# Performance work log

Measured on AMD Instinct MI355X. Metric: run time of the kernel, lower is better.

## Reference

```python
import jax, jax.numpy as jnp
import numpy as np

N_NODES = 50000
N_EDGES = 800000
IN_FEATS = 128
N_HIDDEN = 64
OUT_FEATS = 40
DIM = 8  # pseudo-coordinate dimension
K = 1    # n_kernels


def setup_inputs() -> dict:
    key = jax.random.key(0)
    ks = jax.random.split(key, 12)
    inp = {
        "features": jax.random.normal(ks[0], (N_NODES, IN_FEATS), dtype=jnp.float32),
        "edge_weight": jax.random.normal(ks[1], (N_EDGES, DIM), dtype=jnp.float32),
        "src": jax.random.randint(ks[2], (N_EDGES,), 0, N_NODES),
        "dst": jax.random.randint(ks[3], (N_EDGES,), 0, N_NODES),
        # layer 1 params (fc has no bias in DGL GMMConv; separate additive bias)
        "W1": jax.random.normal(ks[4], (IN_FEATS, K * N_HIDDEN), dtype=jnp.float32) * (1.0 / np.sqrt(IN_FEATS)),
        "b1": jnp.zeros((N_HIDDEN,), dtype=jnp.float32),
        "mu1": jax.random.normal(ks[5], (K, DIM), dtype=jnp.float32) * 0.1,
        "inv_sigma1": jnp.ones((K, DIM), dtype=jnp.float32),
        # layer 2 params
        "W2": jax.random.normal(ks[6], (N_HIDDEN, K * OUT_FEATS), dtype=jnp.float32) * (1.0 / np.sqrt(N_HIDDEN)),
        "b2": jnp.zeros((OUT_FEATS,), dtype=jnp.float32),
        "mu2": jax.random.normal(ks[7], (K, DIM), dtype=jnp.float32) * 0.1,
        "inv_sigma2": jnp.ones((K, DIM), dtype=jnp.float32),
    }
    return inp


def gmm_conv(x, pseudo, src, dst, W, b, mu, inv_sigma, out_feats):
    # x: [N, in], pseudo: [E, DIM], W: [in, K*out]
    h = (x @ W).reshape(-1, K, out_feats)                      # [N, K, out]
    # gaussian mixture weights per edge/kernel: [E, K]
    diff = pseudo[:, None, :] - mu[None, :, :]                 # [E, K, DIM]
    gw = jnp.exp(-0.5 * jnp.sum(diff * diff * (inv_sigma[None] ** 2), axis=-1))
    # gather src feats, weight, sum over kernels: [E, out]
    msg = jnp.einsum("ekf,ek->ef", h[src], gw)
    agg = jax.ops.segment_sum(msg, dst, num_segments=N_NODES)  # [N, out]
    return agg + b


def reference(features, edge_weight, src, dst, W1, b1, mu1, inv_sigma1, W2, b2, mu2, inv_sigma2):
    x = gmm_conv(features, edge_weight, src, dst, W1, b1, mu1, inv_sigma1, N_HIDDEN)
    x = gmm_conv(x, edge_weight, src, dst, W2, b2, mu2, inv_sigma2, OUT_FEATS)
    return jax.nn.log_softmax(x, axis=1)
```

## Files before the change

kernel.cpp:

```cpp
#include <hip/hip_runtime.h>
#include <hip/hip_fp16.h>
#include <math.h>

#define N_NODES 50000
#define N_EDGES 800000
#define IN_FEATS 128
#define N_HIDDEN 64
#define OUT_FEATS 40
#define DIM 8
#define GT_TILES ((N_NODES + 63) / 64)
#define HIST_NB ((N_EDGES / 4 + 255) / 256)
#define FILL_BLOCKS (N_EDGES / 256)
#define SCAN_NB ((N_NODES + 255) / 256)
#define CNT_STRIDE 4

typedef _Float16 half8 __attribute__((ext_vector_type(8)));
typedef float floatx4 __attribute__((ext_vector_type(4)));

__device__ __forceinline__ int wave_incl_scan(int x, int lane) {
#pragma unroll
    for (int off = 1; off < 64; off <<= 1) {
        int v = __shfl_up(x, off, 64);
        if (lane >= off) x += v;
    }
    return x;
}

__global__ __launch_bounds__(256) void histgemm_kernel(
    const float* __restrict__ features, const float* __restrict__ W1,
    const int* __restrict__ dst,
    int* __restrict__ counts, unsigned short* __restrict__ rank,
    __half* __restrict__ h1)
{
    const int tid = threadIdx.x;
    __shared__ __align__(16) __half WT[64][136];

    if (blockIdx.x < HIST_NB) {
        int i = blockIdx.x * 256 + tid;
        if (i * 4 >= N_EDGES) return;
        int4 d = ((const int4*)dst)[i];
        ushort4 r;
        r.x = (unsigned short)atomicAdd(&counts[d.x * CNT_STRIDE], 1);
        r.y = (unsigned short)atomicAdd(&counts[d.y * CNT_STRIDE], 1);
        r.z = (unsigned short)atomicAdd(&counts[d.z * CNT_STRIDE], 1);
        r.w = (unsigned short)atomicAdd(&counts[d.w * CNT_STRIDE], 1);
        ((ushort4*)rank)[i] = r;
        return;
    }

    int nodeBase = (blockIdx.x - HIST_NB) * 64;
    for (int rep = 0; rep < 32; ++rep) {
        int idx = tid + rep * 256;
        int k = idx >> 6, n = idx & 63;
        WT[n][k] = __float2half(W1[idx]);
    }
    __syncthreads();

    int lane = tid & 63, w = tid >> 6;
    int m = lane & 15, quad = lane >> 4;
    int row = nodeBase + w * 16 + m;
    int rowc = (row < N_NODES) ? row : (N_NODES - 1);
    const float* fr = features + (size_t)rowc * IN_FEATS;

    floatx4 acc0 = {0.f,0.f,0.f,0.f}, acc1 = acc0, acc2 = acc0, acc3 = acc0;
#pragma unroll
    for (int kc = 0; kc < 4; ++kc) {
        float4 fa = *(const float4*)(fr + kc * 32 + quad * 8);
        float4 fb = *(const float4*)(fr + kc * 32 + quad * 8 + 4);
        union { half8 v; __half2 h2[4]; } A;
        A.h2[0] = __floats2half2_rn(fa.x, fa.y);
        A.h2[1] = __floats2half2_rn(fa.z, fa.w);
        A.h2[2] = __floats2half2_rn(fb.x, fb.y);
        A.h2[3] = __floats2half2_rn(fb.z, fb.w);
        half8 b0 = *(const half8*)&WT[ 0 + m][kc * 32 + quad * 8];
        half8 b1 = *(const half8*)&WT[16 + m][kc * 32 + quad * 8];
        half8 b2 = *(const half8*)&WT[32 + m][kc * 32 + quad * 8];
        half8 b3 = *(const half8*)&WT[48 + m][kc * 32 + quad * 8];
        acc0 = __builtin_amdgcn_mfma_f32_16x16x32_f16(A.v, b0, acc0, 0, 0, 0);
        acc1 = __builtin_amdgcn_mfma_f32_16x16x32_f16(A.v, b1, acc1, 0, 0, 0);
        acc2 = __builtin_amdgcn_mfma_f32_16x16x32_f16(A.v, b2, acc2, 0, 0, 0);
        acc3 = __builtin_amdgcn_mfma_f32_16x16x32_f16(A.v, b3, acc3, 0, 0, 0);
    }
    int nodeRow = nodeBase + w * 16 + quad * 4;
#pragma unroll
    for (int r = 0; r < 4; ++r) {
        int n = nodeRow + r;
        if (n < N_NODES) {
            size_t base = (size_t)n * N_HIDDEN + m;
            h1[base +  0] = __float2half(acc0[r]);
            h1[base + 16] = __float2half(acc1[r]);
            h1[base + 32] = __float2half(acc2[r]);
            h1[base + 48] = __float2half(acc3[r]);
        }
    }
}

__global__ __launch_bounds__(256) void scan_partial_kernel(const int* __restrict__ counts,
                                                           int* __restrict__ offsets,
                                                           int* __restrict__ partials) {
    const int tid = threadIdx.x, bid = blockIdx.x;
    const int i = bid * 256 + tid;
    const int lane = tid & 63, wid = tid >> 6;
    int x = (i < N_NODES) ? counts[i * CNT_STRIDE] : 0;
    int incl = wave_incl_scan(x, lane);
    __shared__ int wsum[4];
    if (lane == 63) wsum[wid] = incl;
    __syncthreads();
    int base = 0;
#pragma unroll
    for (int w = 0; w < 4; ++w)
        if (w < wid) base += wsum[w];
    if (i < N_NODES) offsets[i] = base + incl - x;
    if (tid == 255) partials[bid] = base + incl;
}

__global__ __launch_bounds__(256) void scan_base_kernel(int* __restrict__ partials) {
    const int tid = threadIdx.x;
    const int lane = tid & 63, wid = tid >> 6;
    int x = (tid < SCAN_NB) ? partials[tid] : 0;
    int incl = wave_incl_scan(x, lane);
    __shared__ int wsum[4];
    if (lane == 63) wsum[wid] = incl;
    __syncthreads();
    int base = 0;
#pragma unroll
    for (int w = 0; w < 4; ++w)
        if (w < wid) base += wsum[w];
    if (tid < SCAN_NB) partials[tid] = base + incl - x;
}

__global__ __launch_bounds__(256) void scan_add_kernel(int* __restrict__ offsets,
                                                       const int* __restrict__ partials) {
    const int i = blockIdx.x * 256 + threadIdx.x;
    if (i < N_NODES) offsets[i] += partials[blockIdx.x];
    if (i == N_NODES) offsets[N_NODES] = N_EDGES;
}

__global__ __launch_bounds__(256) void fill_kernel(
    const int* __restrict__ src, const int* __restrict__ dst,
    const float* __restrict__ ew,
    const float* __restrict__ mu1, const float* __restrict__ is1,
    const float* __restrict__ mu2, const float* __restrict__ is2,
    const int* __restrict__ offsets, const unsigned short* __restrict__ rank,
    int2* __restrict__ csr)
{
    int e = blockIdx.x * 256 + threadIdx.x;
    int sN = src[e];
    int dN = dst[e];
    unsigned short rk = rank[e];
    const float4* ew4 = (const float4*)(ew + (size_t)e * DIM);
    float4 wa = ew4[0], wb = ew4[1];
    float v[8] = {wa.x, wa.y, wa.z, wa.w, wb.x, wb.y, wb.z, wb.w};
    float s1 = 0.f, s2 = 0.f;
#pragma unroll
    for (int d = 0; d < DIM; ++d) {
        float d1 = v[d] - mu1[d]; float a1 = is1[d];
        float d2 = v[d] - mu2[d]; float a2 = is2[d];
        s1 += d1 * d1 * a1 * a1;
        s2 += d2 * d2 * a2 * a2;
    }
    __half2 g = __floats2half2_rn(expf(-0.5f * s1), expf(-0.5f * s2));
    int2 rec;
    rec.x = sN;
    rec.y = *reinterpret_cast<int*>(&g);
    int pos = offsets[dN] + rk;
    __builtin_nontemporal_store(*reinterpret_cast<long long*>(&rec),
                                reinterpret_cast<long long*>(&csr[pos]));
}

__global__ __launch_bounds__(256) void agg1_gemm2_kernel(const __half* __restrict__ h,
                                                         const int* __restrict__ offsets,
                                                         const int2* __restrict__ csr,
                                                         const float* __restrict__ b,
                                                         const float* __restrict__ W2,
                                                         __half* __restrict__ h2) {
    __shared__ float xs[8][64];
    const unsigned* h32 = (const unsigned*)h;
    const int tid = threadIdx.x;
    const int w = tid >> 6, lane = tid & 63;
    const int hf = lane >> 5, p = lane & 31;
    const int ln = w * 2 + hf;
    const int n = blockIdx.x * 8 + ln;
    int beg = offsets[n], end = offsets[n + 1];

    float ax = 0.f, ay = 0.f;
    for (int j = beg; j < end; j += 8) {
        int j0 = j + 0, j1 = j + 1, j2 = j + 2, j3 = j + 3;
        int j4 = j + 4, j5 = j + 5, j6 = j + 6, j7 = j + 7;
        int e1 = end - 1;
        int2 r0 = csr[(j0 < end) ? j0 : e1];
        int2 r1 = csr[(j1 < end) ? j1 : e1];
        int2 r2 = csr[(j2 < end) ? j2 : e1];
        int2 r3 = csr[(j3 < end) ? j3 : e1];
        int2 r4 = csr[(j4 < end) ? j4 : e1];
        int2 r5 = csr[(j5 < end) ? j5 : e1];
        int2 r6 = csr[(j6 < end) ? j6 : e1];
        int2 r7 = csr[(j7 < end) ? j7 : e1];
        unsigned v0 = h32[(size_t)r0.x * 32 + p];
        unsigned v1 = h32[(size_t)r1.x * 32 + p];
        unsigned v2 = h32[(size_t)r2.x * 32 + p];
        unsigned v3 = h32[(size_t)r3.x * 32 + p];
        unsigned v4 = h32[(size_t)r4.x * 32 + p];
        unsigned v5 = h32[(size_t)r5.x * 32 + p];
        unsigned v6 = h32[(size_t)r6.x * 32 + p];
        unsigned v7 = h32[(size_t)r7.x * 32 + p];
        float g0 = (j0 < end) ? __low2float(*reinterpret_cast<__half2*>(&r0.y)) : 0.f;
        float g1 = (j1 < end) ? __low2float(*reinterpret_cast<__half2*>(&r1.y)) : 0.f;
        float g2 = (j2 < end) ? __low2float(*reinterpret_cast<__half2*>(&r2.y)) : 0.f;
        float g3 = (j3 < end) ? __low2float(*reinterpret_cast<__half2*>(&r3.y)) : 0.f;
        float g4 = (j4 < end) ? __low2float(*reinterpret_cast<__half2*>(&r4.y)) : 0.f;
        float g5 = (j5 < end) ? __low2float(*reinterpret_cast<__half2*>(&r5.y)) : 0.f;
        float g6 = (j6 < end) ? __low2float(*reinterpret_cast<__half2*>(&r6.y)) : 0.f;
        float g7 = (j7 < end) ? __low2float(*reinterpret_cast<__half2*>(&r7.y)) : 0.f;
        float2 f0 = __half22float2(*reinterpret_cast<__half2*>(&v0));
        float2 f1 = __half22float2(*reinterpret_cast<__half2*>(&v1));
        float2 f2 = __half22float2(*reinterpret_cast<__half2*>(&v2));
        float2 f3 = __half22float2(*reinterpret_cast<__half2*>(&v3));
        float2 f4 = __half22float2(*reinterpret_cast<__half2*>(&v4));
        float2 f5 = __half22float2(*reinterpret_cast<__half2*>(&v5));
        float2 f6 = __half22float2(*reinterpret_cast<__half2*>(&v6));
        float2 f7 = __half22float2(*reinterpret_cast<__half2*>(&v7));
        ax += f0.x * g0; ay += f0.y * g0;
        ax += f1.x * g1; ay += f1.y * g1;
        ax += f2.x * g2; ay += f2.y * g2;
        ax += f3.x * g3; ay += f3.y * g3;
        ax += f4.x * g4; ay += f4.y * g4;
        ax += f5.x * g5; ay += f5.y * g5;
        ax += f6.x * g6; ay += f6.y * g6;
        ax += f7.x * g7; ay += f7.y * g7;
    }
    float2 bb = *(const float2*)&b[2 * p];
    *(float2*)&xs[ln][2 * p] = make_float2(ax + bb.x, ay + bb.y);
    __syncthreads();

    for (int o = tid; o < 8 * OUT_FEATS; o += 256) {
        int node = o / OUT_FEATS, t = o % OUT_FEATS;
        const float* xr = xs[node];
        float acc = 0.f;
#pragma unroll
        for (int k = 0; k < N_HIDDEN; ++k)
            acc += xr[k] * W2[k * OUT_FEATS + t];
        h2[(size_t)(blockIdx.x * 8 + node) * OUT_FEATS + t] = __float2half(acc);
    }
}

__global__ __launch_bounds__(256) void agg2_kernel(const __half* __restrict__ h,
                                                   const int* __restrict__ offsets,
                                                   const int2* __restrict__ csr,
                                                   const float* __restrict__ b,
                                                   float* __restrict__ out) {
    const unsigned* h32 = (const unsigned*)h;
    const int tid = threadIdx.x;
    const int w = tid >> 6, lane = tid & 63;
    const int hf = lane >> 5, p = lane & 31;
    const int n = blockIdx.x * 8 + w * 2 + hf;
    const int pc = (p < 20) ? p : 19;
    int beg = offsets[n], end = offsets[n + 1];

    float ax = 0.f, ay = 0.f;
    for (int j = beg; j < end; j += 8) {
        int j0 = j + 0, j1 = j + 1, j2 = j + 2, j3 = j + 3;
        int j4 = j + 4, j5 = j + 5, j6 = j + 6, j7 = j + 7;
        int e1 = end - 1;
        int2 r0 = csr[(j0 < end) ? j0 : e1];
        int2 r1 = csr[(j1 < end) ? j1 : e1];
        int2 r2 = csr[(j2 < end) ? j2 : e1];
        int2 r3 = csr[(j3 < end) ? j3 : e1];
        int2 r4 = csr[(j4 < end) ? j4 : e1];
        int2 r5 = csr[(j5 < end) ? j5 : e1];
        int2 r6 = csr[(j6 < end) ? j6 : e1];
        int2 r7 = csr[(j7 < end) ? j7 : e1];
        unsigned v0 = h32[(size_t)r0.x * 20 + pc];
        unsigned v1 = h32[(size_t)r1.x * 20 + pc];
        unsigned v2 = h32[(size_t)r2.x * 20 + pc];
        unsigned v3 = h32[(size_t)r3.x * 20 + pc];
        unsigned v4 = h32[(size_t)r4.x * 20 + pc];
        unsigned v5 = h32[(size_t)r5.x * 20 + pc];
        unsigned v6 = h32[(size_t)r6.x * 20 + pc];
        unsigned v7 = h32[(size_t)r7.x * 20 + pc];
        float g0 = (j0 < end) ? __high2float(*reinterpret_cast<__half2*>(&r0.y)) : 0.f;
        float g1 = (j1 < end) ? __high2float(*reinterpret_cast<__half2*>(&r1.y)) : 0.f;
        float g2 = (j2 < end) ? __high2float(*reinterpret_cast<__half2*>(&r2.y)) : 0.f;
        float g3 = (j3 < end) ? __high2float(*reinterpret_cast<__half2*>(&r3.y)) : 0.f;
        float g4 = (j4 < end) ? __high2float(*reinterpret_cast<__half2*>(&r4.y)) : 0.f;
        float g5 = (j5 < end) ? __high2float(*reinterpret_cast<__half2*>(&r5.y)) : 0.f;
        float g6 = (j6 < end) ? __high2float(*reinterpret_cast<__half2*>(&r6.y)) : 0.f;
        float g7 = (j7 < end) ? __high2float(*reinterpret_cast<__half2*>(&r7.y)) : 0.f;
        float2 f0 = __half22float2(*reinterpret_cast<__half2*>(&v0));
        float2 f1 = __half22float2(*reinterpret_cast<__half2*>(&v1));
        float2 f2 = __half22float2(*reinterpret_cast<__half2*>(&v2));
        float2 f3 = __half22float2(*reinterpret_cast<__half2*>(&v3));
        float2 f4 = __half22float2(*reinterpret_cast<__half2*>(&v4));
        float2 f5 = __half22float2(*reinterpret_cast<__half2*>(&v5));
        float2 f6 = __half22float2(*reinterpret_cast<__half2*>(&v6));
        float2 f7 = __half22float2(*reinterpret_cast<__half2*>(&v7));
        ax += f0.x * g0; ay += f0.y * g0;
        ax += f1.x * g1; ay += f1.y * g1;
        ax += f2.x * g2; ay += f2.y * g2;
        ax += f3.x * g3; ay += f3.y * g3;
        ax += f4.x * g4; ay += f4.y * g4;
        ax += f5.x * g5; ay += f5.y * g5;
        ax += f6.x * g6; ay += f6.y * g6;
        ax += f7.x * g7; ay += f7.y * g7;
    }

    bool valid = (p < 20);
    float vx = valid ? ax + b[2 * p]     : -INFINITY;
    float vy = valid ? ay + b[2 * p + 1] : -INFINITY;
    float m = fmaxf(vx, vy);
#pragma unroll
    for (int off = 16; off; off >>= 1)
        m = fmaxf(m, __shfl_xor(m, off, 32));
    float ex = valid ? (expf(vx - m) + expf(vy - m)) : 0.f;
#pragma unroll
    for (int off = 16; off; off >>= 1)
        ex += __shfl_xor(ex, off, 32);
    float ls = logf(ex);
    if (valid) {
        float2 o = make_float2(vx - m - ls, vy - m - ls);
        *(float2*)&out[(size_t)n * OUT_FEATS + 2 * p] = o;
    }
}

extern "C" void kernel_launch(void* const* d_in, const int* in_sizes, int n_in,
                              void* d_out, int out_size, void* d_ws, size_t ws_size,
                              hipStream_t stream) {
    const float* features    = (const float*)d_in[0];
    const float* edge_weight = (const float*)d_in[1];
    const int*   src         = (const int*)d_in[2];
    const int*   dst         = (const int*)d_in[3];
    const float* W1          = (const float*)d_in[4];
    const float* b1          = (const float*)d_in[5];
    const float* mu1         = (const float*)d_in[6];
    const float* is1         = (const float*)d_in[7];
    const float* W2          = (const float*)d_in[8];
    const float* b2          = (const float*)d_in[9];
    const float* mu2         = (const float*)d_in[10];
    const float* is2         = (const float*)d_in[11];
    float* out = (float*)d_out;

    int2*           csr     = (int2*)d_ws;
    __half*         h1      = (__half*)(csr + N_EDGES);
    __half*         h2      = h1 + (size_t)N_NODES * N_HIDDEN;
    int*            counts  = (int*)(h2 + (size_t)N_NODES * OUT_FEATS);
    unsigned short* rank    = (unsigned short*)(counts + N_NODES * CNT_STRIDE);
    int*            offsets = (int*)(rank + N_EDGES);
    int*            partials= offsets + N_NODES + 1;

    hipMemsetAsync(counts, 0, (size_t)N_NODES * CNT_STRIDE * sizeof(int), stream);

    histgemm_kernel<<<HIST_NB + GT_TILES, 256, 0, stream>>>(
        features, W1, dst, counts, rank, h1);

    scan_partial_kernel<<<SCAN_NB, 256, 0, stream>>>(counts, offsets, partials);
    scan_base_kernel<<<1, 256, 0, stream>>>(partials);
    scan_add_kernel<<<SCAN_NB, 256, 0, stream>>>(offsets, partials);

    fill_kernel<<<FILL_BLOCKS, 256, 0, stream>>>(
        src, dst, edge_weight, mu1, is1, mu2, is2, offsets, rank, csr);

    agg1_gemm2_kernel<<<N_NODES / 8, 256, 0, stream>>>(h1, offsets, csr, b1, W2, h2);

    agg2_kernel<<<N_NODES / 8, 256, 0, stream>>>(h2, offsets, csr, b2, out);
}
```

Baseline: 237.8 us.

## Fold W1·W2 into one projection before first aggregation to shrink gathered rows

Since layer 1 has no nonlinearity, the change precomputes W12 = W1·W2 and the bias term b1·W2 in a small single-block kernel. The first GEMM then projects features straight to 40 columns, and the first aggregation gathers 40-wide rows instead of 64-wide ones, so the per-block GEMM2 and its shared-memory sync go away. This cuts gather bandwidth and the dense work in the aggregation kernel. In exchange it adds a serial single-block kernel launch, and the fp16 rounding of the fused weight changes numerics slightly.

```diff
diff --git a/kernel.cpp b/kernel.cpp
--- a/kernel.cpp
+++ b/kernel.cpp
@@ -13,6 +13,7 @@
 #define FILL_BLOCKS (N_EDGES / 256)
 #define SCAN_NB ((N_NODES + 255) / 256)
 #define CNT_STRIDE 4
+#define WCOLS 48
 
 typedef _Float16 half8 __attribute__((ext_vector_type(8)));
 typedef float floatx4 __attribute__((ext_vector_type(4)));
@@ -26,14 +27,39 @@
     return x;
 }
 
+__global__ __launch_bounds__(256) void w12_kernel(const float* __restrict__ W1,
+                                                  const float* __restrict__ W2,
+                                                  const float* __restrict__ b1,
+                                                  __half* __restrict__ w12T,
+                                                  float* __restrict__ cvec) {
+    const int tid = threadIdx.x;
+    for (int idx = tid; idx < WCOLS * IN_FEATS; idx += 256) {
+        int c = idx >> 7;
+        int i = idx & 127;
+        float s = 0.f;
+        if (c < OUT_FEATS) {
+#pragma unroll 8
+            for (int k = 0; k < N_HIDDEN; ++k)
+                s += W1[i * N_HIDDEN + k] * W2[k * OUT_FEATS + c];
+        }
+        w12T[idx] = __float2half(s);
+    }
+    if (tid < OUT_FEATS) {
+        float s = 0.f;
+        for (int k = 0; k < N_HIDDEN; ++k)
+            s += b1[k] * W2[k * OUT_FEATS + tid];
+        cvec[tid] = s;
+    }
+}
+
 __global__ __launch_bounds__(256) void histgemm_kernel(
-    const float* __restrict__ features, const float* __restrict__ W1,
+    const float* __restrict__ features, const __half* __restrict__ w12T,
     const int* __restrict__ dst,
     int* __restrict__ counts, unsigned short* __restrict__ rank,
-    __half* __restrict__ h1)
+    __half* __restrict__ y)
 {
     const int tid = threadIdx.x;
-    __shared__ __align__(16) __half WT[64][136];
+    __shared__ __align__(16) __half WT[WCOLS][136];
 
     if (blockIdx.x < HIST_NB) {
         int i = blockIdx.x * 256 + tid;
@@ -49,10 +75,9 @@
     }
 
     int nodeBase = (blockIdx.x - HIST_NB) * 64;
-    for (int rep = 0; rep < 32; ++rep) {
+    for (int rep = 0; rep < (WCOLS * IN_FEATS) / 256; ++rep) {
         int idx = tid + rep * 256;
-        int k = idx >> 6, n = idx & 63;
-        WT[n][k] = __float2half(W1[idx]);
+        WT[idx >> 7][idx & 127] = w12T[idx];
     }
     __syncthreads();
 
@@ -62,7 +87,7 @@
     int rowc = (row < N_NODES) ? row : (N_NODES - 1);
     const float* fr = features + (size_t)rowc * IN_FEATS;
 
-    floatx4 acc0 = {0.f,0.f,0.f,0.f}, acc1 = acc0, acc2 = acc0, acc3 = acc0;
+    floatx4 acc0 = {0.f,0.f,0.f,0.f}, acc1 = acc0, acc2 = acc0;
 #pragma unroll
     for (int kc = 0; kc < 4; ++kc) {
         float4 fa = *(const float4*)(fr + kc * 32 + quad * 8);
@@ -75,22 +100,20 @@
         half8 b0 = *(const half8*)&WT[ 0 + m][kc * 32 + quad * 8];
         half8 b1 = *(const half8*)&WT[16 + m][kc * 32 + quad * 8];
         half8 b2 = *(const half8*)&WT[32 + m][kc * 32 + quad * 8];
-        half8 b3 = *(const half8*)&WT[48 + m][kc * 32 + quad * 8];
         acc0 = __builtin_amdgcn_mfma_f32_16x16x32_f16(A.v, b0, acc0, 0, 0, 0);
         acc1 = __builtin_amdgcn_mfma_f32_16x16x32_f16(A.v, b1, acc1, 0, 0, 0);
         acc2 = __builtin_amdgcn_mfma_f32_16x16x32_f16(A.v, b2, acc2, 0, 0, 0);
-        acc3 = __builtin_amdgcn_mfma_f32_16x16x32_f16(A.v, b3, acc3, 0, 0, 0);
     }
     int nodeRow = nodeBase + w * 16 + quad * 4;
 #pragma unroll
     for (int r = 0; r < 4; ++r) {
         int n = nodeRow + r;
         if (n < N_NODES) {
-            size_t base = (size_t)n * N_HIDDEN + m;
-            h1[base +  0] = __float2half(acc0[r]);
-            h1[base + 16] = __float2half(acc1[r]);
-            h1[base + 32] = __float2half(acc2[r]);
-            h1[base + 48] = __float2half(acc3[r]);
+            size_t base = (size_t)n * OUT_FEATS;
+            y[base + m]      = __float2half(acc0[r]);
+            y[base + m + 16] = __float2half(acc1[r]);
+            if (m < 8)
+                y[base + m + 32] = __float2half(acc2[r]);
         }
     }
 }
@@ -168,19 +191,17 @@
                                 reinterpret_cast<long long*>(&csr[pos]));
 }
 
-__global__ __launch_bounds__(256) void agg1_gemm2_kernel(const __half* __restrict__ h,
-                                                         const int* __restrict__ offsets,
-                                                         const int2* __restrict__ csr,
-                                                         const float* __restrict__ b,
-                                                         const float* __restrict__ W2,
-                                                         __half* __restrict__ h2) {
-    __shared__ float xs[8][64];
-    const unsigned* h32 = (const unsigned*)h;
+__global__ __launch_bounds__(256) void agg1_kernel(const __half* __restrict__ ysrc,
+                                                   const int* __restrict__ offsets,
+                                                   const int2* __restrict__ csr,
+                                                   const float* __restrict__ cvec,
+                                                   __half* __restrict__ h2) {
+    const unsigned* h32 = (const unsigned*)ysrc;
     const int tid = threadIdx.x;
     const int w = tid >> 6, lane = tid & 63;
     const int hf = lane >> 5, p = lane & 31;
-    const int ln = w * 2 + hf;
-    const int n = blockIdx.x * 8 + ln;
+    const int n = blockIdx.x * 8 + w * 2 + hf;
+    const int pc = (p < 20) ? p : 19;
     int beg = offsets[n], end = offsets[n + 1];
 
     float ax = 0.f, ay = 0.f;
@@ -196,14 +217,14 @@
         int2 r5 = csr[(j5 < end) ? j5 : e1];
         int2 r6 = csr[(j6 < end) ? j6 : e1];
         int2 r7 = csr[(j7 < end) ? j7 : e1];
-        unsigned v0 = h32[(size_t)r0.x * 32 + p];
-        unsigned v1 = h32[(size_t)r1.x * 32 + p];
-        unsigned v2 = h32[(size_t)r2.x * 32 + p];
-        unsigned v3 = h32[(size_t)r3.x * 32 + p];
-        unsigned v4 = h32[(size_t)r4.x * 32 + p];
-        unsigned v5 = h32[(size_t)r5.x * 32 + p];
-        unsigned v6 = h32[(size_t)r6.x * 32 + p];
-        unsigned v7 = h32[(size_t)r7.x * 32 + p];
+        unsigned v0 = h32[(size_t)r0.x * 20 + pc];
+        unsigned v1 = h32[(size_t)r1.x * 20 + pc];
+        unsigned v2 = h32[(size_t)r2.x * 20 + pc];
+        unsigned v3 = h32[(size_t)r3.x * 20 + pc];
+        unsigned v4 = h32[(size_t)r4.x * 20 + pc];
+        unsigned v5 = h32[(size_t)r5.x * 20 + pc];
+        unsigned v6 = h32[(size_t)r6.x * 20 + pc];
+        unsigned v7 = h32[(size_t)r7.x * 20 + pc];
         float g0 = (j0 < end) ? __low2float(*reinterpret_cast<__half2*>(&r0.y)) : 0.f;
         float g1 = (j1 < end) ? __low2float(*reinterpret_cast<__half2*>(&r1.y)) : 0.f;
         float g2 = (j2 < end) ? __low2float(*reinterpret_cast<__half2*>(&r2.y)) : 0.f;
@@ -229,18 +250,9 @@
         ax += f6.x * g6; ay += f6.y * g6;
         ax += f7.x * g7; ay += f7.y * g7;
     }
-    float2 bb = *(const float2*)&b[2 * p];
-    *(float2*)&xs[ln][2 * p] = make_float2(ax + bb.x, ay + bb.y);
-    __syncthreads();
-
-    for (int o = tid; o < 8 * OUT_FEATS; o += 256) {
-        int node = o / OUT_FEATS, t = o % OUT_FEATS;
-        const float* xr = xs[node];
-        float acc = 0.f;
-#pragma unroll
-        for (int k = 0; k < N_HIDDEN; ++k)
-            acc += xr[k] * W2[k * OUT_FEATS + t];
-        h2[(size_t)(blockIdx.x * 8 + node) * OUT_FEATS + t] = __float2half(acc);
+    if (p < 20) {
+        __half2 hv = __floats2half2_rn(ax + cvec[2 * p], ay + cvec[2 * p + 1]);
+        ((unsigned*)h2)[(size_t)n * 20 + p] = *reinterpret_cast<unsigned*>(&hv);
     }
 }
 
@@ -340,17 +352,21 @@
     float* out = (float*)d_out;
 
     int2*           csr     = (int2*)d_ws;
-    __half*         h1      = (__half*)(csr + N_EDGES);
-    __half*         h2      = h1 + (size_t)N_NODES * N_HIDDEN;
+    __half*         Y       = (__half*)(csr + N_EDGES);
+    __half*         h2      = Y + (size_t)N_NODES * OUT_FEATS;
     int*            counts  = (int*)(h2 + (size_t)N_NODES * OUT_FEATS);
     unsigned short* rank    = (unsigned short*)(counts + N_NODES * CNT_STRIDE);
     int*            offsets = (int*)(rank + N_EDGES);
     int*            partials= offsets + N_NODES + 1;
+    __half*         w12T    = (__half*)(partials + 256);
+    float*          cvec    = (float*)(w12T + WCOLS * IN_FEATS);
 
     hipMemsetAsync(counts, 0, (size_t)N_NODES * CNT_STRIDE * sizeof(int), stream);
 
+    w12_kernel<<<1, 256, 0, stream>>>(W1, W2, b1, w12T, cvec);
+
     histgemm_kernel<<<HIST_NB + GT_TILES, 256, 0, stream>>>(
-        features, W1, dst, counts, rank, h1);
+        features, w12T, dst, counts, rank, Y);
 
     scan_partial_kernel<<<SCAN_NB, 256, 0, stream>>>(counts, offsets, partials);
     scan_base_kernel<<<1, 256, 0, stream>>>(partials);
@@ -359,7 +375,7 @@
     fill_kernel<<<FILL_BLOCKS, 256, 0, stream>>>(
         src, dst, edge_weight, mu1, is1, mu2, is2, offsets, rank, csr);
 
-    agg1_gemm2_kernel<<<N_NODES / 8, 256, 0, stream>>>(h1, offsets, csr, b1, W2, h2);
+    agg1_kernel<<<N_NODES / 8, 256, 0, stream>>>(Y, offsets, csr, cvec, h2);
 
     agg2_kernel<<<N_NODES / 8, 256, 0, stream>>>(h2, offsets, csr, b2, out);
 }
```

Measured after the change: 267.6 us. +12.6%, slower.
